# Optimization experiments

Hardware: AMD Instinct MI355X
Metric: run time of the kernel (lower is better)

Reference implementation:

```python
import jax, jax.numpy as jnp
import numpy as np

B, C, H, W = 16, 1, 128, 8192
N_MAX = 128
CHIRP_W, PERIOD = 48, 64
W_OUT = N_MAX * CHIRP_W + (N_MAX - 1)  # 6271 compacted columns (chirps + separators)
SEP_CLASS_ID = 2


def setup_inputs() -> dict:
    key = jax.random.key(0)
    k1, k2, k3, k4 = jax.random.split(key, 4)
    x = jax.random.normal(k1, (B, C, H, W), dtype=jnp.float32)
    starts = jnp.arange(N_MAX, dtype=jnp.int32) * PERIOD
    xi = jnp.stack([starts, starts + CHIRP_W], axis=-1)           # (N_MAX, 2)
    xi = jnp.broadcast_to(xi[None], (B, N_MAX, 2)).astype(jnp.int32)
    N = jax.random.randint(k2, (B,), 96, N_MAX + 1, dtype=jnp.int32)
    N = N.at[0].set(N_MAX)  # pin so static W_OUT equals torch's dynamic int(w_max.max())
    xl = jax.random.randint(k3, (B, W), 0, 2, dtype=jnp.int32)
    sep_param = jax.random.normal(k4, (1, 1, 1), dtype=jnp.float32)
    return {"x": x, "xi": xi, "N": N, "xl": xl, "sep_param": sep_param, "w_out": W_OUT}


def _compactify(x, xi, N, xl, sep_param, w_out):
    """Vectorized TinyBird.compactify_data: remove silence, keep chirp blocks,
    insert one separator column between consecutive valid chirps."""
    Bx, Cx, Hx, Wx = x.shape
    n_max = xi.shape[1]
    idx = jnp.arange(n_max, dtype=jnp.int32)[None, :]             # (1, N_max)
    Nb = N.reshape(-1, 1).astype(jnp.int32)
    valid = idx < Nb                                              # (B, N_max)

    s0, e0 = xi[..., 0], xi[..., 1]
    w = jnp.clip(e0 - s0, 0, None)
    w_valid = jnp.where(valid, w, 0)
    csum = jnp.cumsum(w_valid, axis=1)
    sn = csum - w_valid + idx                                     # new start (seps before = idx)
    en = csum + idx                                               # new end
    xi_new = jnp.where(valid[..., None], jnp.stack([sn, en], -1), 0).astype(xi.dtype)

    BIG = jnp.int32(1 << 30)
    en_srt = jnp.where(valid, en, BIG)                            # strictly increasing over valid part
    t = jnp.arange(w_out, dtype=jnp.int32)[None, :]               # (1, w_out)
    # i = number of chirp ends <= t  ->  chirp whose [sn_i, en_i) may contain t
    i = (en_srt[:, :, None] <= t[:, None, :]).sum(axis=1).astype(jnp.int32)  # (B, w_out)
    ic = jnp.clip(i, 0, n_max - 1)
    take = lambda a: jnp.take_along_axis(a, ic, axis=1)
    sn_i, en_i = take(sn), take(en)
    s0_i, e0_i = take(s0), take(e0)
    in_chirp = (i < Nb) & (t >= sn_i) & (en_i > sn_i) & (e0_i > s0_i)
    src = jnp.clip(s0_i + (t - sn_i), 0, Wx - 1)                  # (B, w_out)

    # separator column: t == en_{i-1}, previous chirp is not the last valid one, en < W
    jp = jnp.clip(i - 1, 0, n_max - 1)
    en_prev = jnp.take_along_axis(en, jp, axis=1)
    is_sep = (i >= 1) & (t == en_prev) & ((i - 1) < (Nb - 1)) & (en_prev < Wx)

    x_g = jnp.take_along_axis(x, src[:, None, None, :], axis=3)   # (B, C, H, w_out)
    sep = sep_param[0, 0, 0]
    x_new = jnp.where(in_chirp[:, None, None, :], x_g,
                      jnp.where(is_sep[:, None, None, :], sep, jnp.float32(0)))
    xl_g = jnp.take_along_axis(xl, src, axis=1)
    xl_new = jnp.where(in_chirp, xl_g,
                       jnp.where(is_sep, jnp.asarray(SEP_CLASS_ID, xl.dtype),
                                 jnp.asarray(0, xl.dtype)))
    return x_new, xi_new, xl_new


def reference(x, xi, N, xl, sep_param, w_out):
    return _compactify(x, xi, N, xl, sep_param, w_out)
```

## Files before the change

### kernel.cpp

```cpp
#include <hip/hip_runtime.h>

#define BB     16
#define HH     128
#define WW     8192
#define N_MAXC 128
#define W_OUTC 6271
#define SEP_CLASS 2.0f

#define X_ELEMS (BB * HH * W_OUTC)
#define XI_OFF  (X_ELEMS)
#define XL_OFF  (X_ELEMS + BB * N_MAXC * 2)

#define TCOLS 512
#define HROWS 16
#define NTILE 13
#define WS_INTS (BB * 2 * N_MAXC)

typedef float vf4u __attribute__((ext_vector_type(4), aligned(4)));
typedef int   vi4  __attribute__((ext_vector_type(4)));

__device__ __forceinline__ int map_col_lds(int t, int Nb,
                                           const int* s_s0, const int* s_e0,
                                           const int* s_sn, const int* s_en) {
    int lo = 0, hi = Nb;
    while (lo < hi) { int mid = (lo + hi) >> 1; if (s_en[mid] <= t) lo = mid + 1; else hi = mid; }
    const int i  = lo;
    const int ic = (i < N_MAXC - 1) ? i : (N_MAXC - 1);
    if (i < Nb) {
        int sn = s_sn[ic], en = s_en[ic];
        if (t >= sn && en > sn && s_e0[ic] > s_s0[ic]) {
            int src = s_s0[ic] + (t - sn);
            return src < 0 ? 0 : (src > WW - 1 ? WW - 1 : src);
        }
    }
    if (i >= 1) {
        int ep = s_en[i - 1];
        if (t == ep && (i - 1) < (Nb - 1) && ep < WW) return -1;
    }
    return -2;
}

__global__ __launch_bounds__(128) void tb_scan(const int* __restrict__ xi,
                                               const int* __restrict__ Nv,
                                               float* __restrict__ out,
                                               int* __restrict__ ws) {
    __shared__ int s_scan[N_MAXC];
    const int b   = blockIdx.x;
    const int tid = threadIdx.x;
    const int Nb  = Nv[b];
    int2 se = ((const int2*)xi)[b * N_MAXC + tid];
    int w = se.y - se.x; if (w < 0) w = 0;
    const int wv = (tid < Nb) ? w : 0;
    s_scan[tid] = wv;
    __syncthreads();
    #pragma unroll
    for (int off = 1; off < N_MAXC; off <<= 1) {
        int v = (tid >= off) ? s_scan[tid - off] : 0;
        __syncthreads();
        s_scan[tid] += v;
        __syncthreads();
    }
    const int c  = s_scan[tid];
    const int sn = c - wv + tid;
    const int en = c + tid;
    ws[b * 2 * N_MAXC + tid]          = sn;
    ws[b * 2 * N_MAXC + N_MAXC + tid] = en;
    const bool valid = tid < Nb;
    out[XI_OFF + (b * N_MAXC + tid) * 2 + 0] = valid ? (float)sn : 0.0f;
    out[XI_OFF + (b * N_MAXC + tid) * 2 + 1] = valid ? (float)en : 0.0f;
}

__global__ __launch_bounds__(256) void tb_gather(const float* __restrict__ x,
                                                 const int* __restrict__ xi,
                                                 const int* __restrict__ Nv,
                                                 const int* __restrict__ xl,
                                                 const float* __restrict__ sep_param,
                                                 const int* __restrict__ ws,
                                                 float* __restrict__ out) {
    __shared__ int s_sn[N_MAXC], s_en[N_MAXC], s_s0[N_MAXC], s_e0[N_MAXC];
    const int t0  = blockIdx.x * TCOLS;
    const int h0  = blockIdx.y * HROWS;
    const int b   = blockIdx.z;
    const int tid = threadIdx.x;
    const int Nb  = Nv[b];

    if (tid < N_MAXC) {
        s_sn[tid] = ws[b * 2 * N_MAXC + tid];
        s_en[tid] = ws[b * 2 * N_MAXC + N_MAXC + tid];
        int2 se = ((const int2*)xi)[b * N_MAXC + tid];
        s_s0[tid] = se.x; s_e0[tid] = se.y;
    }
    __syncthreads();

    const float sep = sep_param[0];
    const float* xb = x   + ((size_t)b << 20);
    float*       ob = out + (size_t)b * (HH * (size_t)W_OUTC);

    if (blockIdx.y == 0) {
        #pragma unroll
        for (int q = 0; q < 2; ++q) {
            const int t = t0 + tid + q * 256;
            if (t < W_OUTC) {
                const int m = map_col_lds(t, Nb, s_s0, s_e0, s_sn, s_en);
                float v = (m >= 0) ? (float)xl[b * WW + m] : ((m == -1) ? SEP_CLASS : 0.0f);
                out[XL_OFF + b * W_OUTC + t] = v;
            }
        }
    }

    const int c  = tid & 127;
    const int rb = tid >> 7;
    const int tA = t0 + 4 * c;

    int lo = 0, hi = Nb;
    while (lo < hi) { int mid = (lo + hi) >> 1; if (s_en[mid] <= tA) lo = mid + 1; else hi = mid; }
    const int i = lo;
    bool fast = false; int src = 0;
    if (tA + 3 < W_OUTC && i < Nb) {
        const int sn = s_sn[i], en = s_en[i];
        if (tA >= sn && tA + 3 < en && s_e0[i] > s_s0[i]) {
            fast = true;
            src  = s_s0[i] + (tA - sn);
        }
    }

    if (fast) {
        #pragma unroll
        for (int rr = 0; rr < HROWS / 2; ++rr) {
            const int h = h0 + rb + rr * 2;
            const vf4u v = *(const vf4u*)(xb + ((size_t)h << 13) + src);
            *(vf4u*)(ob + (size_t)h * W_OUTC + tA) = v;
        }
    } else {
        int m[4];
        #pragma unroll
        for (int kk = 0; kk < 4; ++kk) {
            const int t = tA + kk;
            m[kk] = (t < W_OUTC) ? map_col_lds(t, Nb, s_s0, s_e0, s_sn, s_en) : -3;
        }
        #pragma unroll
        for (int rr = 0; rr < HROWS / 2; ++rr) {
            const int h = h0 + rb + rr * 2;
            const float* xr   = xb + ((size_t)h << 13);
            float*       orow = ob + (size_t)h * W_OUTC;
            #pragma unroll
            for (int kk = 0; kk < 4; ++kk) {
                const int mm = m[kk];
                if (mm != -3) {
                    orow[tA + kk] = (mm >= 0) ? xr[mm] : ((mm == -1) ? sep : 0.0f);
                }
            }
        }
    }
}

__global__ __launch_bounds__(256, 4) void tb_fused(const float* __restrict__ x,
                                                   const int* __restrict__ xi,
                                                   const int* __restrict__ Nv,
                                                   const int* __restrict__ xl,
                                                   const float* __restrict__ sep_param,
                                                   float* __restrict__ out) {
    __shared__ int s_s0[N_MAXC], s_e0[N_MAXC], s_scan[N_MAXC], s_sn[N_MAXC], s_en[N_MAXC];
    __shared__ __align__(16) int s_map[TCOLS];
    const int t0  = blockIdx.x * TCOLS;
    const int h0  = blockIdx.y * HROWS;
    const int b   = blockIdx.z;
    const int tid = threadIdx.x;
    const int Nb  = Nv[b];
    int wv = 0;
    if (tid < N_MAXC) {
        int2 se = ((const int2*)xi)[b * N_MAXC + tid];
        s_s0[tid] = se.x; s_e0[tid] = se.y;
        int w = se.y - se.x; if (w < 0) w = 0;
        wv = (tid < Nb) ? w : 0;
        s_scan[tid] = wv;
    }
    __syncthreads();
    #pragma unroll
    for (int off = 1; off < N_MAXC; off <<= 1) {
        int v = 0;
        if (tid < N_MAXC && tid >= off) v = s_scan[tid - off];
        __syncthreads();
        if (tid < N_MAXC) s_scan[tid] += v;
        __syncthreads();
    }
    if (tid < N_MAXC) {
        int c = s_scan[tid];
        s_sn[tid] = c - wv + tid;
        s_en[tid] = c + tid;
    }
    __syncthreads();
    #pragma unroll
    for (int q = 0; q < 2; ++q) {
        const int j = tid + q * 256;
        const int t = t0 + j;
        s_map[j] = (t < W_OUTC) ? map_col_lds(t, Nb, s_s0, s_e0, s_sn, s_en) : -2;
    }
    if (blockIdx.y == 0 && blockIdx.x == 0 && tid < N_MAXC) {
        const bool valid = tid < Nb;
        out[XI_OFF + (b * N_MAXC + tid) * 2 + 0] = valid ? (float)s_sn[tid] : 0.0f;
        out[XI_OFF + (b * N_MAXC + tid) * 2 + 1] = valid ? (float)s_en[tid] : 0.0f;
    }
    __syncthreads();
    if (blockIdx.y == 0) {
        #pragma unroll
        for (int q = 0; q < 2; ++q) {
            const int j = tid + q * 256;
            const int t = t0 + j;
            if (t < W_OUTC) {
                const int m = s_map[j];
                float v = (m >= 0) ? (float)xl[b * WW + m] : ((m == -1) ? SEP_CLASS : 0.0f);
                out[XL_OFF + b * W_OUTC + t] = v;
            }
        }
    }
    const float sep = sep_param[0];
    const int   c   = tid & 127;
    const int   rb  = tid >> 7;
    const vi4   mv  = ((const vi4*)s_map)[c];
    const int   tA  = t0 + 4 * c;
    const float* xb = x   + ((size_t)b << 20);
    float*       ob = out + (size_t)b * (HH * W_OUTC);
    const unsigned a0 = (mv.x >= 0) ? (unsigned)mv.x : 0u;
    const unsigned a1 = (mv.y >= 0) ? (unsigned)mv.y : 0u;
    const unsigned a2 = (mv.z >= 0) ? (unsigned)mv.z : 0u;
    const unsigned a3 = (mv.w >= 0) ? (unsigned)mv.w : 0u;
    const float f0 = (mv.x == -1) ? sep : 0.0f;
    const float f1 = (mv.y == -1) ? sep : 0.0f;
    const float f2 = (mv.z == -1) ? sep : 0.0f;
    const float f3 = (mv.w == -1) ? sep : 0.0f;
    if (tA + 3 < W_OUTC) {
        #pragma unroll
        for (int rr = 0; rr < HROWS / 2; ++rr) {
            const int h = h0 + rb + rr * 2;
            const float* xr = xb + ((size_t)h << 13);
            float* orow = ob + (size_t)h * W_OUTC + tA;
            const float v0 = (mv.x >= 0) ? xr[a0] : f0;
            const float v1 = (mv.y >= 0) ? xr[a1] : f1;
            const float v2 = (mv.z >= 0) ? xr[a2] : f2;
            const float v3 = (mv.w >= 0) ? xr[a3] : f3;
            orow[0] = v0; orow[1] = v1; orow[2] = v2; orow[3] = v3;
        }
    } else if (tA < W_OUTC) {
        const int nrem = W_OUTC - tA;
        #pragma unroll
        for (int rr = 0; rr < HROWS / 2; ++rr) {
            const int h = h0 + rb + rr * 2;
            const float* xr = xb + ((size_t)h << 13);
            float* orow = ob + (size_t)h * W_OUTC + tA;
            if (nrem > 0) orow[0] = (mv.x >= 0) ? xr[a0] : f0;
            if (nrem > 1) orow[1] = (mv.y >= 0) ? xr[a1] : f1;
            if (nrem > 2) orow[2] = (mv.z >= 0) ? xr[a2] : f2;
        }
    }
}

extern "C" void kernel_launch(void* const* d_in, const int* in_sizes, int n_in,
                              void* d_out, int out_size, void* d_ws, size_t ws_size,
                              hipStream_t stream) {
    const float* x   = (const float*)d_in[0];
    const int*   xi  = (const int*)  d_in[1];
    const int*   Nv  = (const int*)  d_in[2];
    const int*   xl  = (const int*)  d_in[3];
    const float* sep = (const float*)d_in[4];
    float*       out = (float*)d_out;

    dim3 grid(NTILE, HH / HROWS, BB);

    if (d_ws && ws_size >= WS_INTS * sizeof(int)) {
        int* ws = (int*)d_ws;
        tb_scan<<<dim3(BB), dim3(128), 0, stream>>>(xi, Nv, out, ws);
        tb_gather<<<grid, dim3(256), 0, stream>>>(x, xi, Nv, xl, sep, ws, out);
    } else {
        tb_fused<<<grid, dim3(256), 0, stream>>>(x, xi, Nv, xl, sep, out);
    }
}
```

Before: 140.7 us.

## Restructure gather as chirp-centric copy, tail fill, and label blocks

Replaces the output-column-tiled gather, which binary-searched every column, with a 1D grid of three block roles. Copy blocks take 8 chirps by 16 rows and move each chirp as aligned float4 units, then write the separator columns. Fill blocks zero the tail after the last valid chirp, and aux blocks compute the label row. The aim is to drop the per-column search and scalar fallback paths, at the cost of a hard-coded chirp-width assumption (12 float4 units) and partial-vector handling.

```diff
diff --git a/kernel.cpp b/kernel.cpp
--- a/kernel.cpp
+++ b/kernel.cpp
@@ -11,13 +11,14 @@
 #define XI_OFF  (X_ELEMS)
 #define XL_OFF  (X_ELEMS + BB * N_MAXC * 2)
 
-#define TCOLS 512
-#define HROWS 16
-#define NTILE 13
 #define WS_INTS (BB * 2 * N_MAXC)
 
+#define NCOPY 2048
+#define NFILL 128
+#define NAUX  208
+#define NBLK  (NCOPY + NFILL + NAUX)
+
 typedef float vf4u __attribute__((ext_vector_type(4), aligned(4)));
-typedef int   vi4  __attribute__((ext_vector_type(4)));
 
 __device__ __forceinline__ int map_col_lds(int t, int Nb,
                                            const int* s_s0, const int* s_e0,
@@ -70,89 +71,127 @@
     out[XI_OFF + (b * N_MAXC + tid) * 2 + 1] = valid ? (float)en : 0.0f;
 }
 
-__global__ __launch_bounds__(256) void tb_gather(const float* __restrict__ x,
-                                                 const int* __restrict__ xi,
-                                                 const int* __restrict__ Nv,
-                                                 const int* __restrict__ xl,
-                                                 const float* __restrict__ sep_param,
-                                                 const int* __restrict__ ws,
-                                                 float* __restrict__ out) {
-    __shared__ int s_sn[N_MAXC], s_en[N_MAXC], s_s0[N_MAXC], s_e0[N_MAXC];
-    const int t0  = blockIdx.x * TCOLS;
-    const int h0  = blockIdx.y * HROWS;
-    const int b   = blockIdx.z;
+__global__ __launch_bounds__(256) void tb_main(const float* __restrict__ x,
+                                               const int* __restrict__ xi,
+                                               const int* __restrict__ Nv,
+                                               const int* __restrict__ xl,
+                                               const float* __restrict__ sep_param,
+                                               const int* __restrict__ ws,
+                                               float* __restrict__ out) {
+    __shared__ int s_buf[512];
+    const int bid = blockIdx.x;
     const int tid = threadIdx.x;
-    const int Nb  = Nv[b];
-
-    if (tid < N_MAXC) {
-        s_sn[tid] = ws[b * 2 * N_MAXC + tid];
-        s_en[tid] = ws[b * 2 * N_MAXC + N_MAXC + tid];
-        int2 se = ((const int2*)xi)[b * N_MAXC + tid];
-        s_s0[tid] = se.x; s_e0[tid] = se.y;
-    }
-    __syncthreads();
-
-    const float sep = sep_param[0];
-    const float* xb = x   + ((size_t)b << 20);
-    float*       ob = out + (size_t)b * (HH * (size_t)W_OUTC);
-
-    if (blockIdx.y == 0) {
+
+    if (bid < NCOPY) {
+        const int cg = bid >> 7;
+        const int rg = (bid >> 4) & 7;
+        const int b  = bid & 15;
+        const int Nb = Nv[b];
+        int* s_s0 = s_buf;
+        int* s_sn = s_buf + 8;
+        int* s_w  = s_buf + 16;
+        int* s_sp = s_buf + 24;
+        if (tid < 8) {
+            const int i  = cg * 8 + tid;
+            const int sn = ws[b * 2 * N_MAXC + i];
+            const int en = ws[b * 2 * N_MAXC + N_MAXC + i];
+            int2 se = ((const int2*)xi)[b * N_MAXC + i];
+            int w = se.y - se.x; if (w < 0) w = 0;
+            const bool valid = (i < Nb) && (w > 0);
+            s_s0[tid] = valid ? se.x : 0;
+            s_sn[tid] = valid ? sn   : 0;
+            s_w[tid]  = valid ? w    : 0;
+            s_sp[tid] = (i < Nb - 1 && en < WW) ? en : -1;
+        }
+        __syncthreads();
+
+        const int h0 = rg * 16;
+        const float sep = sep_param[0];
+        const float* xb = x   + ((size_t)(b * HH + h0) << 13);
+        float*       ob = out + (size_t)(b * HH + h0) * W_OUTC;
+
+        unsigned ur[6], us[6], ud[6]; bool ua[6], uf[6]; unsigned uw[6], urem[6];
+        #pragma unroll
+        for (int p = 0; p < 6; ++p) {
+            const unsigned unit = (unsigned)tid + (unsigned)p * 256u;
+            const unsigned r = unit / 96u;
+            const unsigned q = unit - r * 96u;
+            const unsigned j = q / 12u;
+            const unsigned k = q - j * 12u;
+            const unsigned w = (unsigned)s_w[j];
+            ur[p] = r;
+            us[p] = (unsigned)s_s0[j] + 4u * k;
+            ud[p] = (unsigned)s_sn[j] + 4u * k;
+            uw[p] = w;
+            ua[p] = (4u * k < w);
+            uf[p] = (4u * k + 4u <= w);
+            urem[p] = w - 4u * k;
+        }
+        vf4u vv[6];
+        #pragma unroll
+        for (int p = 0; p < 6; ++p) {
+            if (ua[p]) vv[p] = *(const vf4u*)(xb + ((size_t)ur[p] << 13) + us[p]);
+        }
+        #pragma unroll
+        for (int p = 0; p < 6; ++p) {
+            if (uf[p]) {
+                *(vf4u*)(ob + (size_t)ur[p] * W_OUTC + ud[p]) = vv[p];
+            } else if (ua[p]) {
+                float* dd = ob + (size_t)ur[p] * W_OUTC + ud[p];
+                if (urem[p] > 0) dd[0] = vv[p].x;
+                if (urem[p] > 1) dd[1] = vv[p].y;
+                if (urem[p] > 2) dd[2] = vv[p].z;
+            }
+        }
+        if (tid < 128) {
+            const int j = tid >> 4, r = tid & 15;
+            const int pos = s_sp[j];
+            if (pos >= 0) ob[(size_t)r * W_OUTC + pos] = sep;
+        }
+    } else if (bid < NCOPY + NFILL) {
+        const int fid = bid - NCOPY;
+        const int rg  = fid >> 4;
+        const int b   = fid & 15;
+        const int Nb  = Nv[b];
+        int zstart = (Nb > 0) ? ws[b * 2 * N_MAXC + N_MAXC + (Nb - 1)] : 0;
+        if (zstart < 0) zstart = 0;
+        float* ob = out + (size_t)(b * HH + rg * 16) * W_OUTC;
+        for (int r = 0; r < 16; ++r) {
+            float* orow = ob + (size_t)r * W_OUTC;
+            for (int t = zstart + tid; t < W_OUTC; t += 256) orow[t] = 0.0f;
+        }
+    } else {
+        const int aid  = bid - NCOPY - NFILL;
+        const int tile = aid % 13;
+        const int b    = aid / 13;
+        const int Nb   = Nv[b];
+        int* a_s0 = s_buf;
+        int* a_e0 = s_buf + 128;
+        int* a_sn = s_buf + 256;
+        int* a_en = s_buf + 384;
+        if (tid < N_MAXC) {
+            int2 se = ((const int2*)xi)[b * N_MAXC + tid];
+            a_s0[tid] = se.x; a_e0[tid] = se.y;
+            a_sn[tid] = ws[b * 2 * N_MAXC + tid];
+            a_en[tid] = ws[b * 2 * N_MAXC + N_MAXC + tid];
+        }
+        __syncthreads();
         #pragma unroll
         for (int q = 0; q < 2; ++q) {
-            const int t = t0 + tid + q * 256;
+            const int t = tile * 512 + tid + q * 256;
             if (t < W_OUTC) {
-                const int m = map_col_lds(t, Nb, s_s0, s_e0, s_sn, s_en);
+                const int m = map_col_lds(t, Nb, a_s0, a_e0, a_sn, a_en);
                 float v = (m >= 0) ? (float)xl[b * WW + m] : ((m == -1) ? SEP_CLASS : 0.0f);
                 out[XL_OFF + b * W_OUTC + t] = v;
             }
         }
     }
-
-    const int c  = tid & 127;
-    const int rb = tid >> 7;
-    const int tA = t0 + 4 * c;
-
-    int lo = 0, hi = Nb;
-    while (lo < hi) { int mid = (lo + hi) >> 1; if (s_en[mid] <= tA) lo = mid + 1; else hi = mid; }
-    const int i = lo;
-    bool fast = false; int src = 0;
-    if (tA + 3 < W_OUTC && i < Nb) {
-        const int sn = s_sn[i], en = s_en[i];
-        if (tA >= sn && tA + 3 < en && s_e0[i] > s_s0[i]) {
-            fast = true;
-            src  = s_s0[i] + (tA - sn);
-        }
-    }
-
-    if (fast) {
-        #pragma unroll
-        for (int rr = 0; rr < HROWS / 2; ++rr) {
-            const int h = h0 + rb + rr * 2;
-            const vf4u v = *(const vf4u*)(xb + ((size_t)h << 13) + src);
-            *(vf4u*)(ob + (size_t)h * W_OUTC + tA) = v;
-        }
-    } else {
-        int m[4];
-        #pragma unroll
-        for (int kk = 0; kk < 4; ++kk) {
-            const int t = tA + kk;
-            m[kk] = (t < W_OUTC) ? map_col_lds(t, Nb, s_s0, s_e0, s_sn, s_en) : -3;
-        }
-        #pragma unroll
-        for (int rr = 0; rr < HROWS / 2; ++rr) {
-            const int h = h0 + rb + rr * 2;
-            const float* xr   = xb + ((size_t)h << 13);
-            float*       orow = ob + (size_t)h * W_OUTC;
-            #pragma unroll
-            for (int kk = 0; kk < 4; ++kk) {
-                const int mm = m[kk];
-                if (mm != -3) {
-                    orow[tA + kk] = (mm >= 0) ? xr[mm] : ((mm == -1) ? sep : 0.0f);
-                }
-            }
-        }
-    }
-}
+}
+
+#define TCOLS 512
+#define HROWS 16
+#define NTILE 13
+typedef int vi4 __attribute__((ext_vector_type(4)));
 
 __global__ __launch_bounds__(256, 4) void tb_fused(const float* __restrict__ x,
                                                    const int* __restrict__ xi,
@@ -265,13 +304,12 @@
     const float* sep = (const float*)d_in[4];
     float*       out = (float*)d_out;
 
-    dim3 grid(NTILE, HH / HROWS, BB);
-
     if (d_ws && ws_size >= WS_INTS * sizeof(int)) {
         int* ws = (int*)d_ws;
         tb_scan<<<dim3(BB), dim3(128), 0, stream>>>(xi, Nv, out, ws);
-        tb_gather<<<grid, dim3(256), 0, stream>>>(x, xi, Nv, xl, sep, ws, out);
+        tb_main<<<dim3(NBLK), dim3(256), 0, stream>>>(x, xi, Nv, xl, sep, ws, out);
     } else {
+        dim3 grid(NTILE, HH / HROWS, BB);
         tb_fused<<<grid, dim3(256), 0, stream>>>(x, xi, Nv, xl, sep, out);
     }
 }
```

Result: faster. 126.4 us (-10.2%).
